# Kernel optimization log

Hardware: AMD Instinct MI355X
Metric: run time of the kernel (lower is better)

Reference implementation:

```python
import jax, jax.numpy as jnp
import numpy as np

NEG_INF = -jnp.inf

def _sage_conv(x_src, x_dst, src, dst, Wl, bl, Wr, aggr, num_nodes):
    # messages = source features gathered along edges  [E, d]
    msgs = x_src[src]
    if aggr == 'mean':
        s = jax.ops.segment_sum(msgs, dst, num_segments=num_nodes)
        cnt = jax.ops.segment_sum(jnp.ones((src.shape[0],), x_src.dtype), dst, num_segments=num_nodes)
        agg = s / jnp.maximum(cnt, 1.0)[:, None]
    else:  # max; isolated targets -> 0 (PyG scatter-max fill)
        m = jax.ops.segment_max(msgs, dst, num_segments=num_nodes)
        agg = jnp.where(jnp.isfinite(m), m, 0.0)
    return agg @ Wl.T + bl + x_dst @ Wr.T

def setup_inputs() -> dict:
    key = jax.random.key(0)
    ks = jax.random.split(key, 12)
    N, E, D, H, C, L = 40000, 640000, 128, 128, 64, 2
    sc = 0.05
    return {
        'x': jax.random.normal(ks[0], (N, D), jnp.float32),
        'edge_index0': jax.random.randint(ks[1], (2, E), 0, N, jnp.int64),
        'edge_index1': jax.random.randint(ks[2], (2, E), 0, N, jnp.int64),
        'Wl_mean': jax.random.normal(ks[3], (L, H, D), jnp.float32) * sc,
        'bl_mean': jax.random.normal(ks[4], (L, H), jnp.float32) * sc,
        'Wr_mean': jax.random.normal(ks[5], (L, H, D), jnp.float32) * sc,
        'Wl_max': jax.random.normal(ks[6], (L, H, D), jnp.float32) * sc,
        'bl_max': jax.random.normal(ks[7], (L, H), jnp.float32) * sc,
        'Wr_max': jax.random.normal(ks[8], (L, H, D), jnp.float32) * sc,
        'post_W': jax.random.normal(ks[9], (C, 2 * L * H), jnp.float32) * sc,
        'post_b': jax.random.normal(ks[10], (C,), jnp.float32) * sc,
    }

def reference(x, edge_index0, edge_index1, Wl_mean, bl_mean, Wr_mean, Wl_max, bl_max, Wr_max, post_W, post_b):
    N = x.shape[0]
    edge_sets = [edge_index0, edge_index1]
    L = len(edge_sets)
    h = x
    all_layers = []
    for i, ei in enumerate(edge_sets):
        src, dst = ei[0], ei[1]
        x_mean = _sage_conv(h, h, src, dst, Wl_mean[i], bl_mean[i], Wr_mean[i], 'mean', N)
        x_max = _sage_conv(h, h, src, dst, Wl_max[i], bl_max[i], Wr_max[i], 'max', N)
        all_layers.append(x_mean)
        all_layers.append(x_max)
        if i != L - 1:
            h = jax.nn.relu(h)  # note: original never replaces x with conv output
    x_final = jnp.concatenate(all_layers, axis=1) @ post_W.T + post_b
    return jax.nn.log_softmax(x_final, axis=-1)
```

## Files before the change

kernel.cpp:

```cpp
#include <hip/hip_runtime.h>
#include <cstdint>
#include <cstddef>

constexpr int FD = 128;
constexpr int CC = 64;
constexpr int KTOT = 768;
constexpr int CAP = 48;
constexpr int SS = 4096;

typedef __attribute__((ext_vector_type(8))) short short8;
typedef __attribute__((ext_vector_type(4))) float f32x4;

__device__ __forceinline__ float bf2f(unsigned u16) {
  union { unsigned u; float f; } v; v.u = u16 << 16; return v.f;
}
__device__ __forceinline__ unsigned f2bf(float f) {
  union { float f; unsigned u; } v; v.f = f;
  return (v.u + 0x7FFFu + ((v.u >> 16) & 1u)) >> 16;
}
__device__ __forceinline__ unsigned pack2(float a, float b) {
  return f2bf(a) | (f2bf(b) << 16);
}
__device__ __forceinline__ unsigned relu_pk(unsigned v) {
  unsigned m = ((v >> 15) & 0x10001u) * 0xFFFFu;
  return v & ~m;
}

__global__ __launch_bounds__(256) void initpre_kernel(
    const float* __restrict__ x, uint4* __restrict__ xbf4, int n8,
    int* __restrict__ cnt, int ncnt,
    const float* __restrict__ Wl_mean, const float* __restrict__ bl_mean,
    const float* __restrict__ Wr_mean, const float* __restrict__ Wl_max,
    const float* __restrict__ bl_max,  const float* __restrict__ Wr_max,
    const float* __restrict__ postW,   const float* __restrict__ postb,
    unsigned short* __restrict__ Mbf, float* __restrict__ cb)
{
  const int gtid = blockIdx.x * 256 + threadIdx.x;
  const int gsz = gridDim.x * 256;

  for (int t = gtid; t < ncnt; t += gsz) cnt[t] = 0;

  for (int t = gtid; t < n8; t += gsz) {
    float4 a = *(const float4*)(x + (size_t)t * 8);
    float4 b = *(const float4*)(x + (size_t)t * 8 + 4);
    uint4 q;
    q.x = pack2(a.x, a.y); q.y = pack2(a.z, a.w);
    q.z = pack2(b.x, b.y); q.w = pack2(b.z, b.w);
    xbf4[t] = q;
  }

  for (int t = gtid; t < KTOT * CC; t += gsz) {
    int c  = t & (CC - 1);
    int k  = t >> 6;
    int blk = k >> 7;
    int kk  = k & 127;
    const float* pw = postW + (size_t)c * 512;
    float acc = 0.f;
    if (blk < 4) {
      const float* W;
      if (blk == 0)      W = Wl_mean;
      else if (blk == 1) W = Wl_max;
      else if (blk == 2) W = Wl_mean + 128 * 128;
      else               W = Wl_max + 128 * 128;
      const float* pp = pw + blk * 128;
      #pragma unroll 8
      for (int h = 0; h < 128; ++h) acc += pp[h] * W[h * 128 + kk];
    } else if (blk == 4) {
      #pragma unroll 8
      for (int h = 0; h < 128; ++h)
        acc += pw[h] * Wr_mean[h * 128 + kk] + pw[128 + h] * Wr_max[h * 128 + kk];
    } else {
      const float* Wm = Wr_mean + 128 * 128;
      const float* Wx = Wr_max + 128 * 128;
      #pragma unroll 8
      for (int h = 0; h < 128; ++h)
        acc += pw[256 + h] * Wm[h * 128 + kk] + pw[384 + h] * Wx[h * 128 + kk];
    }
    Mbf[(size_t)c * KTOT + k] = (unsigned short)f2bf(acc);

    if (t < CC) {
      const float* pwc = postW + (size_t)t * 512;
      float b = postb[t];
      for (int h = 0; h < 128; ++h) {
        b += bl_mean[h]        * pwc[h]
           + bl_max[h]         * pwc[128 + h]
           + bl_mean[128 + h]  * pwc[256 + h]
           + bl_max[128 + h]   * pwc[384 + h];
      }
      cb[t] = b;
    }
  }
}

__global__ __launch_bounds__(256) void build_kernel(
    const int* __restrict__ e0, int E0,
    const int* __restrict__ e1, int E1,
    int* __restrict__ cnt, unsigned short* __restrict__ csrf, int N, int NC)
{
  const int b = blockIdx.x;
  const int c = b & 7;
  const int t = b >> 3;
  const int nst0 = (E0 + SS - 1) / SS;
  const int* e; int E; int s; int stripe;
  if (t < nst0) { e = e0; E = E0; s = 0; stripe = t; }
  else          { e = e1; E = E1; s = 1; stripe = t - nst0; }
  const int lo = c * NC;
  const int hi = min(N, lo + NC);
  const int i0 = stripe * SS;
  const int i1 = min(E, i0 + SS);
  int* mycnt = cnt + (size_t)(s * 8 + c) * NC;
  unsigned short* mycsr = csrf + (size_t)(s * 8 + c) * NC * CAP;

  for (int i = i0 + threadIdx.x; i < i1; i += 256) {
    int d = e[E + i];
    if (d >= lo && d < hi) {
      int srcv = e[i];
      int n_ = d - lo;
      int pos = atomicAdd(&mycnt[n_], 1);
      if (pos < CAP) mycsr[(size_t)pos * NC + n_] = (unsigned short)srcv;
    }
  }
}

__global__ __launch_bounds__(256) void agg_kernel(
    const unsigned* __restrict__ xbf, const int* __restrict__ cnt,
    const unsigned short* __restrict__ csrf, unsigned* __restrict__ aggbf,
    int N, int NC)
{
  int gw = (blockIdx.x * 256 + threadIdx.x) >> 6;
  int lane = threadIdx.x & 63;
  if (gw >= 2 * N) return;
  const int layer = (gw >= N) ? 1 : 0;
  const int node = gw - layer * N;
  const int cls = node / NC;
  const int n_ = node - cls * NC;
  const int reg = layer * 8 + cls;
  const int deg = min(cnt[(size_t)reg * NC + n_], CAP);
  const unsigned short* cs = csrf + (size_t)reg * NC * CAP + n_;
  const int half = lane >> 5;
  const int hl = lane & 31;
  const float lo = layer ? 0.f : -INFINITY;

  const int n0 = (deg + 1) >> 1;
  const int cbeg = half ? n0 : 0;
  const int ce = half ? deg : n0;

  float s0 = 0.f, s1 = 0.f, s2 = 0.f, s3 = 0.f;
  float m0 = -INFINITY, m1 = -INFINITY, m2 = -INFINITY, m3 = -INFINITY;

  for (int c = cbeg; c < ce; c += 8) {
    int idx[8];
    bool val[8];
    #pragma unroll
    for (int u = 0; u < 8; ++u) {
      int cc = c + u;
      val[u] = cc < ce;
      idx[u] = (int)cs[(size_t)(val[u] ? cc : (ce - 1)) * NC];
    }
    uint2 g[8];
    #pragma unroll
    for (int u = 0; u < 8; ++u)
      g[u] = *(const uint2*)(xbf + (size_t)idx[u] * 64 + hl * 2);
    #pragma unroll
    for (int u = 0; u < 8; ++u) {
      float a0 = fmaxf(bf2f(g[u].x & 0xffffu), lo);
      float a1 = fmaxf(bf2f(g[u].x >> 16), lo);
      float a2 = fmaxf(bf2f(g[u].y & 0xffffu), lo);
      float a3 = fmaxf(bf2f(g[u].y >> 16), lo);
      s0 += val[u] ? a0 : 0.f;  s1 += val[u] ? a1 : 0.f;
      s2 += val[u] ? a2 : 0.f;  s3 += val[u] ? a3 : 0.f;
      m0 = fmaxf(m0, val[u] ? a0 : -INFINITY);
      m1 = fmaxf(m1, val[u] ? a1 : -INFINITY);
      m2 = fmaxf(m2, val[u] ? a2 : -INFINITY);
      m3 = fmaxf(m3, val[u] ? a3 : -INFINITY);
    }
  }

  s0 += __shfl_xor(s0, 32); s1 += __shfl_xor(s1, 32);
  s2 += __shfl_xor(s2, 32); s3 += __shfl_xor(s3, 32);
  m0 = fmaxf(m0, __shfl_xor(m0, 32)); m1 = fmaxf(m1, __shfl_xor(m1, 32));
  m2 = fmaxf(m2, __shfl_xor(m2, 32)); m3 = fmaxf(m3, __shfl_xor(m3, 32));

  if (half == 0) {
    float inv = 1.f / (float)(deg > 0 ? deg : 1);
    if (deg == 0) { m0 = 0.f; m1 = 0.f; m2 = 0.f; m3 = 0.f; }
    unsigned* am = aggbf + (size_t)(layer * 2)     * N * 64;
    unsigned* ax = aggbf + (size_t)(layer * 2 + 1) * N * 64;
    size_t o = (size_t)node * 64 + hl * 2;
    *(uint2*)(am + o) = make_uint2(pack2(s0 * inv, s1 * inv), pack2(s2 * inv, s3 * inv));
    *(uint2*)(ax + o) = make_uint2(pack2(m0, m1), pack2(m2, m3));
  }
}

__global__ __launch_bounds__(256) void gemm_kernel(
    const unsigned* __restrict__ aggbf, const unsigned* __restrict__ xbf,
    const unsigned short* __restrict__ Mbf, const float* __restrict__ cb,
    float* __restrict__ out, int N)
{
  const int tid = threadIdx.x;
  const int w = tid >> 6, l = tid & 63;
  const int l15 = l & 15, lg = l >> 4;
  const int kg = lg * 8;
  const size_t N64 = (size_t)N * 64;
  const int rowb = blockIdx.x * 64 + w * 16;
  const int r0 = rowb + l15;
  const size_t a0r = (size_t)min(r0, N - 1) * 64;

  f32x4 acc[4];
  #pragma unroll
  for (int j = 0; j < 4; ++j) acc[j] = (f32x4){0.f, 0.f, 0.f, 0.f};

  #pragma unroll
  for (int b6 = 0; b6 < 6; ++b6) {
    const unsigned* Ap = (b6 < 4) ? (aggbf + (size_t)b6 * N64) : xbf;
    #pragma unroll
    for (int ss = 0; ss < 4; ++ss) {
      const int k0 = b6 * 128 + ss * 32;
      const int ko = (ss * 32 + kg) >> 1;
      uint4 ua = *(const uint4*)(Ap + a0r + ko);
      if (b6 == 5) {
        ua.x = relu_pk(ua.x); ua.y = relu_pk(ua.y);
        ua.z = relu_pk(ua.z); ua.w = relu_pk(ua.w);
      }
      short8 af = __builtin_bit_cast(short8, ua);
      #pragma unroll
      for (int fc = 0; fc < 4; ++fc) {
        const int c = fc * 16 + l15;
        uint4 qb = *(const uint4*)(Mbf + (size_t)c * KTOT + k0 + kg);
        short8 bf = __builtin_bit_cast(short8, qb);
        acc[fc] = __builtin_amdgcn_mfma_f32_16x16x32_bf16(af, bf, acc[fc], 0, 0, 0);
      }
    }
  }

  float bias[4];
  #pragma unroll
  for (int fc = 0; fc < 4; ++fc) bias[fc] = cb[fc * 16 + l15];

  #pragma unroll
  for (int i = 0; i < 4; ++i) {
    int row = rowb + lg * 4 + i;
    float z0 = acc[0][i] + bias[0];
    float z1 = acc[1][i] + bias[1];
    float z2 = acc[2][i] + bias[2];
    float z3 = acc[3][i] + bias[3];
    float m = fmaxf(fmaxf(z0, z1), fmaxf(z2, z3));
    #pragma unroll
    for (int o = 1; o < 16; o <<= 1) m = fmaxf(m, __shfl_xor(m, o));
    float s = expf(z0 - m) + expf(z1 - m) + expf(z2 - m) + expf(z3 - m);
    #pragma unroll
    for (int o = 1; o < 16; o <<= 1) s += __shfl_xor(s, o);
    float lse = m + logf(s);
    if (row < N) {
      size_t ob = (size_t)row * CC + l15;
      out[ob]      = z0 - lse;
      out[ob + 16] = z1 - lse;
      out[ob + 32] = z2 - lse;
      out[ob + 48] = z3 - lse;
    }
  }
}

extern "C" void kernel_launch(void* const* d_in, const int* in_sizes, int n_in,
                              void* d_out, int out_size, void* d_ws, size_t ws_size,
                              hipStream_t stream)
{
  const float* x       = (const float*)d_in[0];
  const int*   e0      = (const int*)d_in[1];
  const int*   e1      = (const int*)d_in[2];
  const float* Wl_mean = (const float*)d_in[3];
  const float* bl_mean = (const float*)d_in[4];
  const float* Wr_mean = (const float*)d_in[5];
  const float* Wl_max  = (const float*)d_in[6];
  const float* bl_max  = (const float*)d_in[7];
  const float* Wr_max  = (const float*)d_in[8];
  const float* postW   = (const float*)d_in[9];
  const float* postb   = (const float*)d_in[10];
  float* out = (float*)d_out;

  const int N  = in_sizes[0] / FD;
  const int E0 = in_sizes[1] / 2;
  const int E1 = in_sizes[2] / 2;
  const int NC = (N + 7) / 8;

  char* ws = (char*)d_ws;
  size_t off = 0;
  auto alloc = [&](size_t bytes) -> void* {
    void* p = ws + off;
    off = (off + bytes + 255) & ~(size_t)255;
    return p;
  };
  unsigned short* Mbf  = (unsigned short*)alloc((size_t)KTOT * CC * 2);
  float*          cbv  = (float*)alloc(CC * 4);
  int*            cnt  = (int*)alloc((size_t)16 * NC * 4);
  unsigned short* csrf = (unsigned short*)alloc((size_t)16 * NC * CAP * 2);
  unsigned*       xbf  = (unsigned*)alloc((size_t)N * 64 * 4);
  unsigned*       aggbf= (unsigned*)alloc((size_t)4 * N * 64 * 4);
  (void)ws_size; (void)n_in; (void)out_size;

  const int n8 = N * 16;
  initpre_kernel<<<dim3(1024), dim3(256), 0, stream>>>(
      x, (uint4*)xbf, n8, cnt, 16 * NC,
      Wl_mean, bl_mean, Wr_mean, Wl_max, bl_max, Wr_max, postW, postb, Mbf, cbv);

  const int nst = (E0 + SS - 1) / SS + (E1 + SS - 1) / SS;
  build_kernel<<<dim3(8 * nst), dim3(256), 0, stream>>>(
      e0, E0, e1, E1, cnt, csrf, N, NC);

  const int aggBlocks = (2 * N * 64 + 255) / 256;
  agg_kernel<<<dim3(aggBlocks), dim3(256), 0, stream>>>(xbf, cnt, csrf, aggbf, N, NC);

  gemm_kernel<<<dim3((N + 63) / 64), dim3(256), 0, stream>>>(
      aggbf, xbf, Mbf, cbv, out, N);
}
```

Before: 275.3 us.

## Precompute ReLU'd bf16 features and simplify aggregation inner loop arithmetic

The init kernel now writes a second bf16 copy of x with ReLU already applied. Both the layer-1 gather and the GEMM read this copy, which removes the per-element clamp and mask work. The aggregation loop uses 32-bit byte offsets, clamps padded slots to the last valid neighbor instead of predicating each accumulate, and subtracts the padded contributions from the sum afterwards. This cuts ALU work in the gather loop at the cost of an extra N×128 bf16 buffer write, and the padding correction adds small rounding differences to the mean.

```diff
diff --git a/kernel.cpp b/kernel.cpp
--- a/kernel.cpp
+++ b/kernel.cpp
@@ -11,8 +11,8 @@
 typedef __attribute__((ext_vector_type(8))) short short8;
 typedef __attribute__((ext_vector_type(4))) float f32x4;
 
-__device__ __forceinline__ float bf2f(unsigned u16) {
-  union { unsigned u; float f; } v; v.u = u16 << 16; return v.f;
+__device__ __forceinline__ float u2f(unsigned u) {
+  union { unsigned u; float f; } v; v.u = u; return v.f;
 }
 __device__ __forceinline__ unsigned f2bf(float f) {
   union { float f; unsigned u; } v; v.f = f;
@@ -27,8 +27,8 @@
 }
 
 __global__ __launch_bounds__(256) void initpre_kernel(
-    const float* __restrict__ x, uint4* __restrict__ xbf4, int n8,
-    int* __restrict__ cnt, int ncnt,
+    const float* __restrict__ x, uint4* __restrict__ xbf4, uint4* __restrict__ xrbf4,
+    int n8, int* __restrict__ cnt, int ncnt,
     const float* __restrict__ Wl_mean, const float* __restrict__ bl_mean,
     const float* __restrict__ Wr_mean, const float* __restrict__ Wl_max,
     const float* __restrict__ bl_max,  const float* __restrict__ Wr_max,
@@ -47,6 +47,10 @@
     q.x = pack2(a.x, a.y); q.y = pack2(a.z, a.w);
     q.z = pack2(b.x, b.y); q.w = pack2(b.z, b.w);
     xbf4[t] = q;
+    uint4 r;
+    r.x = relu_pk(q.x); r.y = relu_pk(q.y);
+    r.z = relu_pk(q.z); r.w = relu_pk(q.w);
+    xrbf4[t] = r;
   }
 
   for (int t = gtid; t < KTOT * CC; t += gsz) {
@@ -123,9 +127,9 @@
 }
 
 __global__ __launch_bounds__(256) void agg_kernel(
-    const unsigned* __restrict__ xbf, const int* __restrict__ cnt,
-    const unsigned short* __restrict__ csrf, unsigned* __restrict__ aggbf,
-    int N, int NC)
+    const unsigned* __restrict__ xbf, const unsigned* __restrict__ xrbf,
+    const int* __restrict__ cnt, const unsigned short* __restrict__ csrf,
+    unsigned* __restrict__ aggbf, int N, int NC)
 {
   int gw = (blockIdx.x * 256 + threadIdx.x) >> 6;
   int lane = threadIdx.x & 63;
@@ -136,43 +140,57 @@
   const int n_ = node - cls * NC;
   const int reg = layer * 8 + cls;
   const int deg = min(cnt[(size_t)reg * NC + n_], CAP);
-  const unsigned short* cs = csrf + (size_t)reg * NC * CAP + n_;
+  const char* csb = (const char*)(csrf + (size_t)reg * NC * CAP);
+  const char* xl  = (const char*)(layer ? xrbf : xbf);
   const int half = lane >> 5;
   const int hl = lane & 31;
-  const float lo = layer ? 0.f : -INFINITY;
+  const unsigned lb = (unsigned)hl * 8u;
 
   const int n0 = (deg + 1) >> 1;
   const int cbeg = half ? n0 : 0;
-  const int ce = half ? deg : n0;
+  const int ce   = half ? deg : n0;
+  const int cnth = ce - cbeg;
+  const unsigned strideB = (unsigned)NC * 2u;
 
   float s0 = 0.f, s1 = 0.f, s2 = 0.f, s3 = 0.f;
   float m0 = -INFINITY, m1 = -INFINITY, m2 = -INFINITY, m3 = -INFINITY;
 
-  for (int c = cbeg; c < ce; c += 8) {
-    int idx[8];
-    bool val[8];
-    #pragma unroll
-    for (int u = 0; u < 8; ++u) {
-      int cc = c + u;
-      val[u] = cc < ce;
-      idx[u] = (int)cs[(size_t)(val[u] ? cc : (ce - 1)) * NC];
-    }
-    uint2 g[8];
-    #pragma unroll
-    for (int u = 0; u < 8; ++u)
-      g[u] = *(const uint2*)(xbf + (size_t)idx[u] * 64 + hl * 2);
-    #pragma unroll
-    for (int u = 0; u < 8; ++u) {
-      float a0 = fmaxf(bf2f(g[u].x & 0xffffu), lo);
-      float a1 = fmaxf(bf2f(g[u].x >> 16), lo);
-      float a2 = fmaxf(bf2f(g[u].y & 0xffffu), lo);
-      float a3 = fmaxf(bf2f(g[u].y >> 16), lo);
-      s0 += val[u] ? a0 : 0.f;  s1 += val[u] ? a1 : 0.f;
-      s2 += val[u] ? a2 : 0.f;  s3 += val[u] ? a3 : 0.f;
-      m0 = fmaxf(m0, val[u] ? a0 : -INFINITY);
-      m1 = fmaxf(m1, val[u] ? a1 : -INFINITY);
-      m2 = fmaxf(m2, val[u] ? a2 : -INFINITY);
-      m3 = fmaxf(m3, val[u] ? a3 : -INFINITY);
+  if (cnth > 0) {
+    unsigned off = (unsigned)cbeg * strideB + (unsigned)n_ * 2u;
+    const unsigned omax = (unsigned)(ce - 1) * strideB + (unsigned)n_ * 2u;
+    const int niter = (cnth + 7) >> 3;
+    for (int it = 0; it < niter; ++it) {
+      unsigned o[8];
+      #pragma unroll
+      for (int u = 0; u < 8; ++u) o[u] = min(off + (unsigned)u * strideB, omax);
+      off += 8u * strideB;
+      unsigned idx[8];
+      #pragma unroll
+      for (int u = 0; u < 8; ++u) idx[u] = *(const unsigned short*)(csb + o[u]);
+      uint2 g[8];
+      #pragma unroll
+      for (int u = 0; u < 8; ++u)
+        g[u] = *(const uint2*)(xl + ((idx[u] << 8) + lb));
+      #pragma unroll
+      for (int u = 0; u < 8; ++u) {
+        float a0 = u2f(g[u].x << 16);
+        float a1 = u2f(g[u].x & 0xffff0000u);
+        float a2 = u2f(g[u].y << 16);
+        float a3 = u2f(g[u].y & 0xffff0000u);
+        s0 += a0; s1 += a1; s2 += a2; s3 += a3;
+        m0 = fmaxf(m0, a0); m1 = fmaxf(m1, a1);
+        m2 = fmaxf(m2, a2); m3 = fmaxf(m3, a3);
+      }
+    }
+    const int npad = niter * 8 - cnth;
+    if (npad > 0) {
+      unsigned idx = *(const unsigned short*)(csb + omax);
+      uint2 g = *(const uint2*)(xl + ((idx << 8) + lb));
+      float fn = (float)npad;
+      s0 = fmaf(-fn, u2f(g.x << 16), s0);
+      s1 = fmaf(-fn, u2f(g.x & 0xffff0000u), s1);
+      s2 = fmaf(-fn, u2f(g.y << 16), s2);
+      s3 = fmaf(-fn, u2f(g.y & 0xffff0000u), s3);
     }
   }
 
@@ -194,6 +212,7 @@
 
 __global__ __launch_bounds__(256) void gemm_kernel(
     const unsigned* __restrict__ aggbf, const unsigned* __restrict__ xbf,
+    const unsigned* __restrict__ xrbf,
     const unsigned short* __restrict__ Mbf, const float* __restrict__ cb,
     float* __restrict__ out, int N)
 {
@@ -212,16 +231,13 @@
 
   #pragma unroll
   for (int b6 = 0; b6 < 6; ++b6) {
-    const unsigned* Ap = (b6 < 4) ? (aggbf + (size_t)b6 * N64) : xbf;
+    const unsigned* Ap = (b6 < 4) ? (aggbf + (size_t)b6 * N64)
+                                  : (b6 == 4 ? xbf : xrbf);
     #pragma unroll
     for (int ss = 0; ss < 4; ++ss) {
       const int k0 = b6 * 128 + ss * 32;
       const int ko = (ss * 32 + kg) >> 1;
       uint4 ua = *(const uint4*)(Ap + a0r + ko);
-      if (b6 == 5) {
-        ua.x = relu_pk(ua.x); ua.y = relu_pk(ua.y);
-        ua.z = relu_pk(ua.z); ua.w = relu_pk(ua.w);
-      }
       short8 af = __builtin_bit_cast(short8, ua);
       #pragma unroll
       for (int fc = 0; fc < 4; ++fc) {
@@ -295,12 +311,13 @@
   int*            cnt  = (int*)alloc((size_t)16 * NC * 4);
   unsigned short* csrf = (unsigned short*)alloc((size_t)16 * NC * CAP * 2);
   unsigned*       xbf  = (unsigned*)alloc((size_t)N * 64 * 4);
+  unsigned*       xrbf = (unsigned*)alloc((size_t)N * 64 * 4);
   unsigned*       aggbf= (unsigned*)alloc((size_t)4 * N * 64 * 4);
   (void)ws_size; (void)n_in; (void)out_size;
 
   const int n8 = N * 16;
   initpre_kernel<<<dim3(1024), dim3(256), 0, stream>>>(
-      x, (uint4*)xbf, n8, cnt, 16 * NC,
+      x, (uint4*)xbf, (uint4*)xrbf, n8, cnt, 16 * NC,
       Wl_mean, bl_mean, Wr_mean, Wl_max, bl_max, Wr_max, postW, postb, Mbf, cbv);
 
   const int nst = (E0 + SS - 1) / SS + (E1 + SS - 1) / SS;
@@ -308,8 +325,9 @@
       e0, E0, e1, E1, cnt, csrf, N, NC);
 
   const int aggBlocks = (2 * N * 64 + 255) / 256;
-  agg_kernel<<<dim3(aggBlocks), dim3(256), 0, stream>>>(xbf, cnt, csrf, aggbf, N, NC);
+  agg_kernel<<<dim3(aggBlocks), dim3(256), 0, stream>>>(
+      xbf, xrbf, cnt, csrf, aggbf, N, NC);
 
   gemm_kernel<<<dim3((N + 63) / 64), dim3(256), 0, stream>>>(
-      aggbf, xbf, Mbf, cbv, out, N);
-}
+      aggbf, xbf, xrbf, Mbf, cbv, out, N);
+}
```

New measurement: 262.1 us. -4.8%, faster.
